# Kernel optimization log

Measured on AMD Instinct MI355X. Metric: run time of the kernel, lower is better.

Reference implementation:

```python
import jax, jax.numpy as jnp
import numpy as np

B, T, OBS, H, A, S = 4096, 64, 64, 64, 8, 201


def setup_inputs() -> dict:
    key = jax.random.key(0)
    ks = jax.random.split(key, 13)
    n = lambda k, shp, s=1.0: jax.random.normal(k, shp, dtype=jnp.float32) * s
    return {
        "x": n(ks[0], (B, T, OBS)),
        "stack": jnp.zeros((B, S, H), jnp.float32),
        "stack_ptrs": jax.random.randint(ks[1], (B, 1), 0, 100, dtype=jnp.int32),
        # core_network: init.normal_(std=1.0) per source
        "W1": n(ks[2], (H, OBS + H)), "b1": n(ks[3], (H,)),
        "W2": n(ks[4], (H, H)), "b2": n(ks[5], (H,)),
        # stack_head: default torch Linear init ~ U(-1/sqrt(H), 1/sqrt(H))
        "Ws": (jax.random.uniform(ks[6], (3, H), dtype=jnp.float32) * 2 - 1) / np.sqrt(H),
        "bs": (jax.random.uniform(ks[7], (3,), dtype=jnp.float32) * 2 - 1) / np.sqrt(H),
        # policy/value heads: init.normal_(std=0.01)
        "Wp": n(ks[8], (A, H), 0.01), "bp": n(ks[9], (A,), 0.01),
        "Wv": n(ks[10], (1, H), 0.01), "bv": n(ks[11], (1,), 0.01),
    }


def reference(x, stack, stack_ptrs, W1, b1, W2, b2, Ws, bs, Wp, bp, Wv, bv):
    # x: [B,T,OBS]  stack: [B,S,H]  stack_ptrs: [B,1] int
    batch = x.shape[0]
    bidx = jnp.arange(batch)
    ptrs0 = stack_ptrs.astype(jnp.int32)[:, 0]  # [B]

    def step(carry, x_t):
        stk, ptrs = carry
        top = stk[bidx, ptrs]                                   # [B,H] gather at ptr
        h = jnp.tanh(jnp.concatenate([x_t, top], axis=1) @ W1.T + b1)
        p = jnp.tanh(h @ W2.T + b2)                             # [B,H]
        probs = jax.nn.softmax(p @ Ws.T + bs, axis=1)           # [B,3]
        ops = jnp.argmax(probs, axis=1).astype(jnp.int32)       # 0=pop,1=noop,2=push
        push = (ops == 2)[:, None]
        # conditional scatter: write p at row ptr only where op==2
        stk = stk.at[bidx, ptrs].set(jnp.where(push, p, top))
        ptrs = jnp.maximum(ptrs + ops - 1, 0)
        logits = p @ Wp.T + bp                                  # [B,A]
        value = (p @ Wv.T + bv)[:, 0]                           # [B]
        return (stk, ptrs), (logits, value)

    (stack_out, ptrs_out), (logits_t, values_t) = jax.lax.scan(
        step, (stack, ptrs0), jnp.swapaxes(x, 0, 1))
    logitss = jnp.swapaxes(logits_t, 0, 1)      # [B,T,A]
    values = values_t.reshape(-1)               # time-major [T*B], matching torch layout
    return logitss, values, stack_out, ptrs_out[:, None]
```

## Files before the change

### kernel.cpp

```cpp
#include <hip/hip_runtime.h>
#include <cstddef>

#define NB 4096
#define NT 64
#define NOBS 64
#define NH 64
#define NA 8
#define NS 201


__global__ void copy_stack_kernel(const float4* __restrict__ src,
                                  float4* __restrict__ dst, int n4) {
    int i = blockIdx.x * blockDim.x + threadIdx.x;
    if (i < n4) dst[i] = src[i];
}

__launch_bounds__(256, 2)
__global__ void stacknet_kernel(const float* __restrict__ x,
                                const int* __restrict__ ptrs_in,
                                const float* __restrict__ W1,
                                const float* __restrict__ b1,
                                const float* __restrict__ W2,
                                const float* __restrict__ b2,
                                const float* __restrict__ Ws,
                                const float* __restrict__ bs,
                                const float* __restrict__ Wp,
                                const float* __restrict__ bp,
                                const float* __restrict__ Wv,
                                const float* __restrict__ bv,
                                float* __restrict__ logits_out,
                                float* __restrict__ values_out,
                                float* __restrict__ stack,
                                float* __restrict__ ptrs_out) {
    const int lane = threadIdx.x & 63;
    const int wv = threadIdx.x >> 6;
    const int b = (blockIdx.x << 2) + wv;
    const int aa = lane & 15;

    __shared__ __align__(16) float shw[16 * 68];
    __shared__ float shb[16];
    __shared__ __align__(16) float vbuf[4][256];

    for (int i = threadIdx.x; i < 16 * 64; i += 256) {
        int a = i >> 6, k = i & 63;
        float w = 0.0f;
        if (a < 3)        w = Ws[a * 64 + k];
        else if (a < 11)  w = Wp[(a - 3) * 64 + k];
        else if (a == 11) w = Wv[k];
        shw[a * 68 + k] = w;
    }
    if (threadIdx.x < 16) {
        int a = threadIdx.x;
        float bb = 0.0f;
        if (a < 3) bb = bs[a];
        else if (a < 11) bb = bp[a - 3];
        else if (a == 11) bb = bv[0];
        shb[a] = bb;
    }
    __syncthreads();

    float w1r[128];
#pragma unroll
    for (int j = 0; j < 32; ++j) {
        float4 tW = ((const float4*)W1)[lane * 32 + j];
        w1r[4*j] = tW.x; w1r[4*j+1] = tW.y; w1r[4*j+2] = tW.z; w1r[4*j+3] = tW.w;
    }
    float w2r[64];
#pragma unroll
    for (int j = 0; j < 16; ++j) {
        float4 tW = ((const float4*)W2)[lane * 16 + j];
        w2r[4*j] = tW.x; w2r[4*j+1] = tW.y; w2r[4*j+2] = tW.z; w2r[4*j+3] = tW.w;
    }
    float b1r = b1[lane];
    float b2r = b2[lane];

    int ptr = ptrs_in[b];
    const float* xb  = x + (size_t)b * NT * NOBS;
    float* stk       = stack + (size_t)b * NS * NH;
    float* lgb       = logits_out + (size_t)b * NT * NA;

    float* v = &vbuf[wv][0];
    const float* shwa = &shw[aa * 68];
    const float shba = shb[aa];

    float top = stk[ptr * 64 + lane];
    bool pushed = false;
    float pushval = 0.0f;

    for (int t = 0; t < NT; ++t) {
        int r0 = (ptr > 0) ? (ptr - 1) : 0;
        float c0 = stk[r0 * 64 + lane];
        float c2 = stk[(ptr + 1) * 64 + lane];
        float xv = xb[t * 64 + lane];

        v[lane]      = xv;
        v[64 + lane] = top;

        float acc = 0.0f;
        const float4* v4 = (const float4*)v;
#pragma unroll
        for (int j = 0; j < 32; ++j) {
            float4 a4 = v4[j];
            acc = fmaf(w1r[4*j],   a4.x, acc);
            acc = fmaf(w1r[4*j+1], a4.y, acc);
            acc = fmaf(w1r[4*j+2], a4.z, acc);
            acc = fmaf(w1r[4*j+3], a4.w, acc);
        }
        float h = tanhf(acc + b1r);
        v[128 + lane] = h;

        float acc2 = 0.0f;
        const float4* h4 = (const float4*)(v + 128);
#pragma unroll
        for (int j = 0; j < 16; ++j) {
            float4 a4 = h4[j];
            acc2 = fmaf(w2r[4*j],   a4.x, acc2);
            acc2 = fmaf(w2r[4*j+1], a4.y, acc2);
            acc2 = fmaf(w2r[4*j+2], a4.z, acc2);
            acc2 = fmaf(w2r[4*j+3], a4.w, acc2);
        }
        float p = tanhf(acc2 + b2r);
        v[192 + lane] = p;

        float hacc = 0.0f;
        const float4* p4 = (const float4*)(v + 192);
#pragma unroll
        for (int j = 0; j < 16; ++j) {
            float4 w4 = *(const float4*)(shwa + 4*j);
            float4 a4 = p4[j];
            hacc = fmaf(a4.x, w4.x, hacc);
            hacc = fmaf(a4.y, w4.y, hacc);
            hacc = fmaf(a4.z, w4.z, hacc);
            hacc = fmaf(a4.w, w4.w, hacc);
        }
        float sv = hacc + shba;

        float s0 = __shfl(sv, 0, 64), s1 = __shfl(sv, 1, 64), s2 = __shfl(sv, 2, 64);
        float m = fmaxf(fmaxf(s0, s1), s2);
        float e0 = expf(s0 - m), e1 = expf(s1 - m), e2 = expf(s2 - m);
        float S = (e0 + e1) + e2;
        float p0 = e0 / S, p1 = e1 / S, p2 = e2 / S;
        int op = 0; float pm = p0;
        if (p1 > pm) { pm = p1; op = 1; }
        if (p2 > pm) { op = 2; }

        if (op == 2) stk[ptr * 64 + lane] = p;

        float sel = (op == 0) ? (pushed ? pushval : c0)
                              : ((op == 1) ? top : c2);
        pushed = (op == 2);
        pushval = p;

        int np = ptr + op - 1;
        ptr = (np < 0) ? 0 : np;
        top = sel;

        if (lane >= 3 && lane <= 10) {
            lgb[t * NA + (lane - 3)] = sv;
        }
        if (lane == 11) {
            values_out[(size_t)t * NB + b] = sv;
        }
    }
    if (lane == 0) ptrs_out[b] = (float)ptr;
}

extern "C" void kernel_launch(void* const* d_in, const int* in_sizes, int n_in,
                              void* d_out, int out_size, void* d_ws, size_t ws_size,
                              hipStream_t stream) {
    const float* x        = (const float*)d_in[0];
    const float* stack_in = (const float*)d_in[1];
    const int*   ptrs_in  = (const int*)d_in[2];
    const float* W1 = (const float*)d_in[3];
    const float* b1 = (const float*)d_in[4];
    const float* W2 = (const float*)d_in[5];
    const float* b2 = (const float*)d_in[6];
    const float* Ws = (const float*)d_in[7];
    const float* bs = (const float*)d_in[8];
    const float* Wp = (const float*)d_in[9];
    const float* bp = (const float*)d_in[10];
    const float* Wv = (const float*)d_in[11];
    const float* bv = (const float*)d_in[12];

    float* out      = (float*)d_out;
    float* logits   = out;
    float* values   = out + 2097152;
    float* stack    = out + 2359296;
    float* ptrs_out = out + 55050240;

    int n4 = 52690944 / 4;
    copy_stack_kernel<<<51456, 256, 0, stream>>>((const float4*)stack_in,
                                                 (float4*)stack, n4);
    stacknet_kernel<<<1024, 256, 0, stream>>>(x, ptrs_in, W1, b1, W2, b2,
                                              Ws, bs, Wp, bp, Wv, bv,
                                              logits, values, stack, ptrs_out);
}
```

Measured before the change: 742.8 us.

## Fuse stack copy into recurrent kernel and read x directly via scalar loads

Removes the separate stack-copy kernel launch: each wavefront now copies its own batch row of the stack from input to output before running the recurrence. The x_t input is read directly from global memory with a wave-uniform address (readfirstlane on the wave index), so it can use scalar loads and no longer needs staging through LDS. The LDS vector buffer shrinks accordingly. The trade-off is that the 200MB copy now runs inside the latency-bound kernel, which has only 1024 blocks, instead of in a wide, bandwidth-saturating grid, so copy throughput may drop. Each wave reads back stack rows it just wrote itself, without an explicit fence.

Result: slower. 835.0 us (+12.4%).

```diff
diff --git a/kernel.cpp b/kernel.cpp
--- a/kernel.cpp
+++ b/kernel.cpp
@@ -9,14 +9,10 @@
 #define NS 201
 
 
-__global__ void copy_stack_kernel(const float4* __restrict__ src,
-                                  float4* __restrict__ dst, int n4) {
-    int i = blockIdx.x * blockDim.x + threadIdx.x;
-    if (i < n4) dst[i] = src[i];
-}
 
 __launch_bounds__(256, 2)
 __global__ void stacknet_kernel(const float* __restrict__ x,
+                                const float* __restrict__ stack_in,
                                 const int* __restrict__ ptrs_in,
                                 const float* __restrict__ W1,
                                 const float* __restrict__ b1,
@@ -33,13 +29,21 @@
                                 float* __restrict__ stack,
                                 float* __restrict__ ptrs_out) {
     const int lane = threadIdx.x & 63;
-    const int wv = threadIdx.x >> 6;
+    const int wv = __builtin_amdgcn_readfirstlane(threadIdx.x >> 6);
     const int b = (blockIdx.x << 2) + wv;
     const int aa = lane & 15;
 
+    float* stk = stack + (size_t)b * NS * NH;
+
+    {
+        const float4* s4 = (const float4*)(stack_in + (size_t)b * NS * NH);
+        float4* d4 = (float4*)stk;
+        for (int i = lane; i < (NS * NH / 4); i += 64) d4[i] = s4[i];
+    }
+
     __shared__ __align__(16) float shw[16 * 68];
     __shared__ float shb[16];
-    __shared__ __align__(16) float vbuf[4][256];
+    __shared__ __align__(16) float vbuf[4][192];
 
     for (int i = threadIdx.x; i < 16 * 64; i += 256) {
         int a = i >> 6, k = i & 63;
@@ -75,9 +79,8 @@
     float b2r = b2[lane];
 
     int ptr = ptrs_in[b];
-    const float* xb  = x + (size_t)b * NT * NOBS;
-    float* stk       = stack + (size_t)b * NS * NH;
-    float* lgb       = logits_out + (size_t)b * NT * NA;
+    const float* xb = x + (size_t)b * NT * NOBS;
+    float* lgb      = logits_out + (size_t)b * NT * NA;
 
     float* v = &vbuf[wv][0];
     const float* shwa = &shw[aa * 68];
@@ -91,26 +94,28 @@
         int r0 = (ptr > 0) ? (ptr - 1) : 0;
         float c0 = stk[r0 * 64 + lane];
         float c2 = stk[(ptr + 1) * 64 + lane];
-        float xv = xb[t * 64 + lane];
-
-        v[lane]      = xv;
-        v[64 + lane] = top;
-
+
+        v[lane] = top;
+
+        const float* xt = xb + t * 64;
         float acc = 0.0f;
+#pragma unroll
+        for (int k = 0; k < 64; ++k)
+            acc = fmaf(w1r[k], xt[k], acc);
         const float4* v4 = (const float4*)v;
 #pragma unroll
-        for (int j = 0; j < 32; ++j) {
+        for (int j = 0; j < 16; ++j) {
             float4 a4 = v4[j];
-            acc = fmaf(w1r[4*j],   a4.x, acc);
-            acc = fmaf(w1r[4*j+1], a4.y, acc);
-            acc = fmaf(w1r[4*j+2], a4.z, acc);
-            acc = fmaf(w1r[4*j+3], a4.w, acc);
+            acc = fmaf(w1r[64 + 4*j],   a4.x, acc);
+            acc = fmaf(w1r[64 + 4*j+1], a4.y, acc);
+            acc = fmaf(w1r[64 + 4*j+2], a4.z, acc);
+            acc = fmaf(w1r[64 + 4*j+3], a4.w, acc);
         }
         float h = tanhf(acc + b1r);
-        v[128 + lane] = h;
+        v[64 + lane] = h;
 
         float acc2 = 0.0f;
-        const float4* h4 = (const float4*)(v + 128);
+        const float4* h4 = (const float4*)(v + 64);
 #pragma unroll
         for (int j = 0; j < 16; ++j) {
             float4 a4 = h4[j];
@@ -120,10 +125,10 @@
             acc2 = fmaf(w2r[4*j+3], a4.w, acc2);
         }
         float p = tanhf(acc2 + b2r);
-        v[192 + lane] = p;
+        v[128 + lane] = p;
 
         float hacc = 0.0f;
-        const float4* p4 = (const float4*)(v + 192);
+        const float4* p4 = (const float4*)(v + 128);
 #pragma unroll
         for (int j = 0; j < 16; ++j) {
             float4 w4 = *(const float4*)(shwa + 4*j);
@@ -188,10 +193,8 @@
     float* stack    = out + 2359296;
     float* ptrs_out = out + 55050240;
 
-    int n4 = 52690944 / 4;
-    copy_stack_kernel<<<51456, 256, 0, stream>>>((const float4*)stack_in,
-                                                 (float4*)stack, n4);
-    stacknet_kernel<<<1024, 256, 0, stream>>>(x, ptrs_in, W1, b1, W2, b2,
+    stacknet_kernel<<<1024, 256, 0, stream>>>(x, stack_in, ptrs_in,
+                                              W1, b1, W2, b2,
                                               Ws, bs, Wp, bp, Wv, bv,
                                               logits, values, stack, ptrs_out);
 }
```
